# Performance work log

Measured on AMD Instinct MI355X. Metric: run time of the kernel, lower is better.

Reference implementation:

```python
import jax, jax.numpy as jnp
import numpy as np

B, L, D, H = 2, 2048, 1024, 16
DH = D // H
NEG = -10000.0

def setup_inputs() -> dict:
    key = jax.random.key(0)
    ks = jax.random.split(key, 6)
    scale = 1.0 / np.sqrt(D)
    inp = {
        "x": jax.random.normal(ks[0], (B, L, D), dtype=jnp.float32),
        "m": jnp.ones((B, L), dtype=jnp.int32),  # 1 = valid token, 0 = padded
        "Wq": jax.random.normal(ks[1], (D, D), dtype=jnp.float32) * scale,
        "bq": jnp.zeros((D,), dtype=jnp.float32),
        "Wk": jax.random.normal(ks[2], (D, D), dtype=jnp.float32) * scale,
        "bk": jnp.zeros((D,), dtype=jnp.float32),
        "Wv": jax.random.normal(ks[3], (D, D), dtype=jnp.float32) * scale,
        "bv": jnp.zeros((D,), dtype=jnp.float32),
        "Wp": jax.random.normal(ks[4], (D, D), dtype=jnp.float32) * scale,
        "bp": jnp.zeros((D,), dtype=jnp.float32),
    }
    return inp

def reference(x, m, Wq, bq, Wk, bk, Wv, bv, Wp, bp):
    # torch Linear: x @ W.T + b
    def heads(t):  # (B,L,D) -> (B,H,L,DH)
        return t.reshape(B, L, H, DH).transpose(0, 2, 1, 3)
    q = heads(x @ Wq.T + bq)
    k = heads(x @ Wk.T + bk)
    v = heads(x @ Wv.T + bv)
    att = jnp.einsum("bhqd,bhkd->bhqk", q, k) * (1.0 / np.sqrt(DH))  # (B,H,L,L)
    causal = jnp.tril(jnp.ones((L, L), dtype=bool))[None, None]       # (1,1,L,L)
    att = jnp.where(causal, att, NEG)
    # additive key-padding mask: 0 for valid, -10000 for padded keys
    pad = (1.0 - m.astype(att.dtype))[:, None, None, :] * NEG         # (B,1,1,L)
    att = att + pad
    att = jax.nn.softmax(att, axis=-1)
    y = jnp.einsum("bhqk,bhkd->bhqd", att, v)                          # (B,H,L,DH)
    y = y.transpose(0, 2, 1, 3).reshape(B, L, D)
    return y @ Wp.T + bp
```

## Files before the change

### kernel.cpp

```cpp
#include <hip/hip_runtime.h>
#include <hip/hip_bf16.h>

#define NB 2
#define NL 2048
#define ND 1024
#define NH 16
#define NDH 64
#define NM (NB*NL)

typedef unsigned short u16;
typedef __attribute__((ext_vector_type(8))) short short8;
typedef __attribute__((ext_vector_type(4))) float floatx4;

#define QSCALE 0.180336880f

__device__ __forceinline__ u16 f2bf(float f) {
  union { float f; unsigned int u; } v; v.f = f;
  unsigned int r = v.u + 0x7FFF + ((v.u >> 16) & 1);
  return (u16)(r >> 16);
}

__device__ __forceinline__ void async_cp16(const u16* lds, const u16* g) {
  __builtin_amdgcn_global_load_lds(
      (const __attribute__((address_space(1))) void*)g,
      (__attribute__((address_space(3))) void*)lds, 16, 0, 0);
}

__device__ __forceinline__ float dpp_xor1_f(float v) {
  return __int_as_float(__builtin_amdgcn_mov_dpp(__float_as_int(v), 0xB1, 0xF, 0xF, true));
}

__device__ __forceinline__ unsigned pk_bf16(float lo, float hi) {
  __hip_bfloat162 h2 = __float22bfloat162_rn(make_float2(lo, hi));
  return *(unsigned*)&h2;
}

__global__ __launch_bounds__(256)
void cvt_all(const float* __restrict__ wq, const float* __restrict__ wk,
             const float* __restrict__ wv, const float* __restrict__ wp,
             const float* __restrict__ x,
             u16* __restrict__ ow, u16* __restrict__ ox)
{
  const int per4 = ND * ND / 4;
  const int tot  = 4 * per4 + NM * ND / 4;
  for (int t = blockIdx.x * 256 + threadIdx.x; t < tot; t += gridDim.x * 256) {
    const float* src; uint2* dst; int off;
    if (t < 4 * per4) {
      int w = t >> 18; off = t & (per4 - 1);
      src = (w == 0) ? wq : (w == 1) ? wk : (w == 2) ? wv : wp;
      dst = (uint2*)(ow + (size_t)w * ND * ND);
    } else {
      off = t - 4 * per4; src = x; dst = (uint2*)ox;
    }
    float4 f = ((const float4*)src)[off];
    u16 h[4] = { f2bf(f.x), f2bf(f.y), f2bf(f.z), f2bf(f.w) };
    dst[off] = *(const uint2*)h;
  }
}

#define BM 128
#define BN 128
#define BK 32
#define LDT 32

__global__ __launch_bounds__(256)
void gemm_qkv(const u16* __restrict__ A, const u16* __restrict__ Wb,
              const float* __restrict__ bq, const float* __restrict__ bk,
              const float* __restrict__ bv,
              u16* __restrict__ Qb, u16* __restrict__ Kb, u16* __restrict__ Vb)
{
  const int n0g = blockIdx.x * BN;
  const int z   = n0g >> 10;
  const int n0  = n0g & 1023;
  const u16* W    = Wb + (size_t)z * ND * ND;
  const float* Bi = (z == 0) ? bq : (z == 1) ? bk : bv;
  u16* C          = (z == 0) ? Qb : (z == 1) ? Kb : Vb;
  const float sc  = (z == 0) ? QSCALE : 1.0f;

  const int m0 = blockIdx.y * BM;
  const int tid  = threadIdx.x;
  const int lane = tid & 63;
  const int wave = tid >> 6;
  const int wm = (wave >> 1) * 64;
  const int wn = (wave & 1) * 64;
  const int quad = lane >> 4;
  const int l16  = lane & 15;

  __shared__ u16 As[BM * LDT];
  __shared__ u16 Bs[BN * LDT];

  floatx4 acc[4][4];
#pragma unroll
  for (int i = 0; i < 4; ++i)
#pragma unroll
    for (int j = 0; j < 4; ++j)
      acc[i][j] = (floatx4){0.f, 0.f, 0.f, 0.f};

  for (int k0 = 0; k0 < ND; k0 += BK) {
#pragma unroll
    for (int it = 0; it < 2; ++it) {
      int idx = tid + it * 256;
      int rr  = idx >> 2;
      int c8  = (idx & 3) << 3;
      async_cp16(&Bs[idx * 8], &W[(size_t)(n0 + rr) * ND + k0 + c8]);
      async_cp16(&As[idx * 8], &A[(size_t)(m0 + rr) * ND + k0 + c8]);
    }
    __syncthreads();

    short8 af[4], bfr[4];
#pragma unroll
    for (int i = 0; i < 4; ++i)
      af[i] = *(const short8*)&As[(wm + i * 16 + l16) * LDT + quad * 8];
#pragma unroll
    for (int j = 0; j < 4; ++j)
      bfr[j] = *(const short8*)&Bs[(wn + j * 16 + l16) * LDT + quad * 8];

#pragma unroll
    for (int i = 0; i < 4; ++i)
#pragma unroll
      for (int j = 0; j < 4; ++j)
        acc[i][j] = __builtin_amdgcn_mfma_f32_16x16x32_bf16(af[i], bfr[j], acc[i][j], 0, 0, 0);
    __syncthreads();
  }

#pragma unroll
  for (int j = 0; j < 4; ++j) {
    const int ncol = n0 + wn + j * 16 + l16;
    const float bv2 = Bi[ncol];
#pragma unroll
    for (int i = 0; i < 4; ++i) {
      const int mbase = m0 + wm + i * 16 + quad * 4;
#pragma unroll
      for (int r2 = 0; r2 < 4; ++r2) {
        float v = (acc[i][j][r2] + bv2) * sc;
        C[(size_t)(mbase + r2) * ND + ncol] = f2bf(v);
      }
    }
  }
}

#define BN2 64

__global__ __launch_bounds__(256)
void gemm_proj(const u16* __restrict__ A, const u16* __restrict__ W,
               const float* __restrict__ Bi, float* __restrict__ C)
{
  const int n0 = blockIdx.x * BN2;
  const int m0 = blockIdx.y * BM;
  const int tid  = threadIdx.x;
  const int lane = tid & 63;
  const int wave = tid >> 6;
  const int wm = (wave >> 1) * 64;
  const int wn = (wave & 1) * 32;
  const int quad = lane >> 4;
  const int l16  = lane & 15;

  __shared__ u16 As[BM * LDT];
  __shared__ u16 Bs[BN2 * LDT];

  floatx4 acc[4][2];
#pragma unroll
  for (int i = 0; i < 4; ++i)
#pragma unroll
    for (int j = 0; j < 2; ++j)
      acc[i][j] = (floatx4){0.f, 0.f, 0.f, 0.f};

  for (int k0 = 0; k0 < ND; k0 += BK) {
#pragma unroll
    for (int it = 0; it < 2; ++it) {
      int idx = tid + it * 256;
      int rr  = idx >> 2;
      int c8  = (idx & 3) << 3;
      async_cp16(&As[idx * 8], &A[(size_t)(m0 + rr) * ND + k0 + c8]);
    }
    {
      int rr = tid >> 2, c8 = (tid & 3) << 3;
      async_cp16(&Bs[tid * 8], &W[(size_t)(n0 + rr) * ND + k0 + c8]);
    }
    __syncthreads();

    short8 af[4], bfr[2];
#pragma unroll
    for (int i = 0; i < 4; ++i)
      af[i] = *(const short8*)&As[(wm + i * 16 + l16) * LDT + quad * 8];
#pragma unroll
    for (int j = 0; j < 2; ++j)
      bfr[j] = *(const short8*)&Bs[(wn + j * 16 + l16) * LDT + quad * 8];

#pragma unroll
    for (int i = 0; i < 4; ++i)
#pragma unroll
      for (int j = 0; j < 2; ++j)
        acc[i][j] = __builtin_amdgcn_mfma_f32_16x16x32_bf16(af[i], bfr[j], acc[i][j], 0, 0, 0);
    __syncthreads();
  }

#pragma unroll
  for (int j = 0; j < 2; ++j) {
    const int ncol = n0 + wn + j * 16 + l16;
    const float bv2 = Bi[ncol];
#pragma unroll
    for (int i = 0; i < 4; ++i) {
      const int mbase = m0 + wm + i * 16 + quad * 4;
#pragma unroll
      for (int r2 = 0; r2 < 4; ++r2)
        C[(size_t)(mbase + r2) * ND + ncol] = acc[i][j][r2] + bv2;
    }
  }
}

#define TSTR 66
__global__ __launch_bounds__(256)
void vtrans(const u16* __restrict__ V, u16* __restrict__ VT)
{
  const int lt = blockIdx.x;
  const int bh = blockIdx.y;
  const int b = bh >> 4, h = bh & 15;
  const int l0 = lt * 64;
  const int tid = threadIdx.x;
  __shared__ u16 Ls[64][TSTR];
#pragma unroll
  for (int p = 0; p < 2; ++p) {
    int idx = tid + p * 256;
    int r = idx >> 3, c = (idx & 7) << 3;
    *(uint4*)&Ls[r][c] = *(const uint4*)&V[(size_t)(b * NL + l0 + r) * ND + h * NDH + c];
  }
  __syncthreads();
#pragma unroll
  for (int p = 0; p < 2; ++p) {
    int idx = tid + p * 256;
    int lg = idx & 7, d = idx >> 3;
    u16 tb[8];
#pragma unroll
    for (int e = 0; e < 8; ++e) tb[e] = Ls[lg * 8 + e][d];
    *(uint4*)&VT[((size_t)(b * NH + h) * NDH + d) * NL + l0 + lg * 8] = *(const uint4*)tb;
  }
}

#define KC 64
#define PSTR 72

__global__ __launch_bounds__(256)
void attn_mfma(const u16* __restrict__ Q, const u16* __restrict__ K,
               const u16* __restrict__ VT, const int* __restrict__ msk,
               u16* __restrict__ Y)
{
  const int t = blockIdx.x;
  const int r = t >> 8;
  const int xcd = t & 7;
  const int v = (t >> 3) & 31;
  const int bh = xcd * 4 + r;
  const int qt = (r == 0) ? v
               : (r == 1) ? 31 - v
               : (r == 2) ? ((v + 16) & 31)
                          : ((15 - v) & 31);
  const int b = bh >> 4;
  const int h = bh & 15;
  const int q0 = qt * 64;
  const int tid  = threadIdx.x;
  const int lane = tid & 63;
  const int wave = tid >> 6;
  const int wq   = wave * 16;
  const int quad = lane >> 4;
  const int l16  = lane & 15;

  __shared__ u16 Ks[KC * 64];
  __shared__ u16 Vt[NDH * 64];
  __shared__ u16 Ps[64][PSTR];
  __shared__ u16 Ms[NL];

  const int nchunks = qt + 1;

  for (int j = tid; j < nchunks * KC; j += 256) Ms[j] = (u16)(msk[b * NL + j] ? 1 : 0);

  const u16* Kbase  = K  + (size_t)b * NL * ND + h * NDH;
  const u16* VTbase = VT + (size_t)(b * NH + h) * NDH * NL;

  short8 qf[2];
#pragma unroll
  for (int kk = 0; kk < 2; ++kk)
    qf[kk] = *(const short8*)&Q[(size_t)(b * NL + q0 + wq + l16) * ND
                                + h * NDH + kk * 32 + quad * 8];

  short8 onesf;
  {
    const short ov = (l16 == 0) ? (short)0x3F80 : (short)0;
#pragma unroll
    for (int e = 0; e < 8; ++e) onesf[e] = ov;
  }

  floatx4 o[4];
#pragma unroll
  for (int ot = 0; ot < 4; ++ot) o[ot] = (floatx4){0.f, 0.f, 0.f, 0.f};
  floatx4 lacc = (floatx4){0.f, 0.f, 0.f, 0.f};

  const int odd = l16 & 1;
  const int sw  = l16 & 7;

  for (int kc = 0; kc < nchunks; ++kc) {
    const int k0 = kc * KC;

#pragma unroll
    for (int p = 0; p < 2; ++p) {
      int sl = tid + p * 256;
      int rr = sl >> 3;
      int ch = (sl & 7) ^ (rr & 7);
      async_cp16(&Ks[sl * 8], Kbase + (size_t)(k0 + rr) * ND + ch * 8);
      async_cp16(&Vt[sl * 8], VTbase + (size_t)rr * NL + k0 + ch * 8);
    }
    __syncthreads();

    floatx4 sc[4];
#pragma unroll
    for (int ct = 0; ct < 4; ++ct) {
      const u16* krow = &Ks[(ct * 16 + l16) * 64];
      short8 kf0 = *(const short8*)(krow + ((quad ^ sw) << 3));
      short8 kf1 = *(const short8*)(krow + (((4 | quad) ^ sw) << 3));
      floatx4 a = (floatx4){0.f, 0.f, 0.f, 0.f};
      a = __builtin_amdgcn_mfma_f32_16x16x32_bf16(qf[0], kf0, a, 0, 0, 0);
      a = __builtin_amdgcn_mfma_f32_16x16x32_bf16(qf[1], kf1, a, 0, 0, 0);
      sc[ct] = a;
    }

    const bool diag = (kc == qt);
    const int rowb = q0 + wq + quad * 4;
#pragma unroll
    for (int ct = 0; ct < 4; ++ct) {
      const int col = k0 + ct * 16 + l16;
      const float pmul = (float)Ms[col];
      float pv[4];
#pragma unroll
      for (int r2 = 0; r2 < 4; ++r2) {
        float p = pmul * __builtin_amdgcn_exp2f(sc[ct][r2]);
        if (diag) p = (col > rowb + r2) ? 0.f : p;
        pv[r2] = p;
      }
      float nb0 = dpp_xor1_f(pv[0]), nb1 = dpp_xor1_f(pv[1]);
      float nb2 = dpp_xor1_f(pv[2]), nb3 = dpp_xor1_f(pv[3]);
      const int colb  = ct * 16 + (l16 & ~1);
      const int row01 = wq + quad * 4 + odd;
      unsigned d01 = odd ? pk_bf16(nb1, pv[1]) : pk_bf16(pv[0], nb0);
      unsigned d23 = odd ? pk_bf16(nb3, pv[3]) : pk_bf16(pv[2], nb2);
      *(unsigned*)&Ps[row01][colb]     = d01;
      *(unsigned*)&Ps[row01 + 2][colb] = d23;
    }

#pragma unroll
    for (int kk = 0; kk < 2; ++kk) {
      short8 pf = *(const short8*)&Ps[wq + l16][kk * 32 + quad * 8];
#pragma unroll
      for (int ot = 0; ot < 4; ++ot) {
        const u16* vrow = &Vt[(ot * 16 + l16) * 64];
        short8 vf = *(const short8*)(vrow + ((((kk << 2) | quad) ^ sw) << 3));
        o[ot] = __builtin_amdgcn_mfma_f32_16x16x32_bf16(pf, vf, o[ot], 0, 0, 0);
      }
      lacc = __builtin_amdgcn_mfma_f32_16x16x32_bf16(pf, onesf, lacc, 0, 0, 0);
    }
    __syncthreads();
  }

  float inv[4];
#pragma unroll
  for (int r2 = 0; r2 < 4; ++r2) {
    const float l = __shfl(lacc[r2], quad << 4);
    inv[r2] = 1.0f / l;
  }
#pragma unroll
  for (int ot = 0; ot < 4; ++ot)
#pragma unroll
    for (int r2 = 0; r2 < 4; ++r2) {
      const int row = q0 + wq + quad * 4 + r2;
      Y[(size_t)(b * NL + row) * ND + h * NDH + ot * 16 + l16] = f2bf(o[ot][r2] * inv[r2]);
    }
}

extern "C" void kernel_launch(void* const* d_in, const int* in_sizes, int n_in,
                              void* d_out, int out_size, void* d_ws, size_t ws_size,
                              hipStream_t stream) {
  const float* x  = (const float*)d_in[0];
  const int*   m  = (const int*)d_in[1];
  const float* Wq = (const float*)d_in[2];
  const float* bq = (const float*)d_in[3];
  const float* Wk = (const float*)d_in[4];
  const float* bk = (const float*)d_in[5];
  const float* Wv = (const float*)d_in[6];
  const float* bv = (const float*)d_in[7];
  const float* Wp = (const float*)d_in[8];
  const float* bp = (const float*)d_in[9];
  float* out = (float*)d_out;

  const size_t per = (size_t)NM * ND;
  u16* Qb = (u16*)d_ws;
  u16* Kb = Qb + per;
  u16* Vb = Kb + per;
  u16* Wb = Vb + per;
  u16* Yb = Qb;
  u16* xb = (u16*)d_out;
  u16* VTb = xb + per;

  cvt_all<<<2048, 256, 0, stream>>>(Wq, Wk, Wv, Wp, x, Wb, xb);

  gemm_qkv<<<dim3(3 * ND / BN, NM / BM), 256, 0, stream>>>(
      xb, Wb, bq, bk, bv, Qb, Kb, Vb);

  vtrans<<<dim3(NL / 64, NB * NH), 256, 0, stream>>>(Vb, VTb);

  attn_mfma<<<1024, 256, 0, stream>>>(Qb, Kb, VTb, m, Yb);

  const u16* Wpb = Wb + 3 * (size_t)ND * ND;
  gemm_proj<<<dim3(ND / BN2, NM / BM), 256, 0, stream>>>(Yb, Wpb, bp, out);
}
```

Measured before the change: 195.5 us.

## Fuse V transpose into QKV GEMM epilogue, deepen proj K tile, stream mask

The QKV GEMM epilogue now writes the V projection directly in transposed head-major layout with packed 4-element stores, which removes the separate vtrans kernel and its extra read and write of V. The output projection GEMM doubles its K tile to 64, halving barrier count per K loop. The attention kernel drops the LDS mask staging, reads the mask from global per chunk, and splits the diagonal chunk out of the loop so the causal compare is specialised away. The transposed V writes are strided 8-byte stores, which may be less coalesced than the old transpose kernel's writes.

```diff
diff --git a/kernel.cpp b/kernel.cpp
--- a/kernel.cpp
+++ b/kernel.cpp
@@ -67,14 +67,13 @@
 void gemm_qkv(const u16* __restrict__ A, const u16* __restrict__ Wb,
               const float* __restrict__ bq, const float* __restrict__ bk,
               const float* __restrict__ bv,
-              u16* __restrict__ Qb, u16* __restrict__ Kb, u16* __restrict__ Vb)
+              u16* __restrict__ Qb, u16* __restrict__ Kb, u16* __restrict__ VTb)
 {
   const int n0g = blockIdx.x * BN;
   const int z   = n0g >> 10;
   const int n0  = n0g & 1023;
   const u16* W    = Wb + (size_t)z * ND * ND;
   const float* Bi = (z == 0) ? bq : (z == 1) ? bk : bv;
-  u16* C          = (z == 0) ? Qb : (z == 1) ? Kb : Vb;
   const float sc  = (z == 0) ? QSCALE : 1.0f;
 
   const int m0 = blockIdx.y * BM;
@@ -123,23 +122,43 @@
     __syncthreads();
   }
 
-#pragma unroll
-  for (int j = 0; j < 4; ++j) {
-    const int ncol = n0 + wn + j * 16 + l16;
-    const float bv2 = Bi[ncol];
-#pragma unroll
-    for (int i = 0; i < 4; ++i) {
-      const int mbase = m0 + wm + i * 16 + quad * 4;
-#pragma unroll
-      for (int r2 = 0; r2 < 4; ++r2) {
-        float v = (acc[i][j][r2] + bv2) * sc;
-        C[(size_t)(mbase + r2) * ND + ncol] = f2bf(v);
+  if (z == 2) {
+#pragma unroll
+    for (int j = 0; j < 4; ++j) {
+      const int ncol = n0 + wn + j * 16 + l16;
+      const int h2 = ncol >> 6, d = ncol & 63;
+      const float bv2 = Bi[ncol];
+#pragma unroll
+      for (int i = 0; i < 4; ++i) {
+        const int mbase = m0 + wm + i * 16 + quad * 4;
+        const int b2 = mbase >> 11, l = mbase & (NL - 1);
+        uint2 val;
+        val.x = pk_bf16(acc[i][j][0] + bv2, acc[i][j][1] + bv2);
+        val.y = pk_bf16(acc[i][j][2] + bv2, acc[i][j][3] + bv2);
+        *(uint2*)&VTb[((size_t)(b2 * NH + h2) * NDH + d) * NL + l] = val;
       }
     }
+  } else {
+    u16* C = (z == 0) ? Qb : Kb;
+#pragma unroll
+    for (int j = 0; j < 4; ++j) {
+      const int ncol = n0 + wn + j * 16 + l16;
+      const float bv2 = Bi[ncol];
+#pragma unroll
+      for (int i = 0; i < 4; ++i) {
+        const int mbase = m0 + wm + i * 16 + quad * 4;
+#pragma unroll
+        for (int r2 = 0; r2 < 4; ++r2) {
+          float v = (acc[i][j][r2] + bv2) * sc;
+          C[(size_t)(mbase + r2) * ND + ncol] = f2bf(v);
+        }
+      }
+    }
   }
 }
 
 #define BN2 64
+#define BK2 64
 
 __global__ __launch_bounds__(256)
 void gemm_proj(const u16* __restrict__ A, const u16* __restrict__ W,
@@ -155,8 +174,8 @@
   const int quad = lane >> 4;
   const int l16  = lane & 15;
 
-  __shared__ u16 As[BM * LDT];
-  __shared__ u16 Bs[BN2 * LDT];
+  __shared__ u16 As[BM * BK2];
+  __shared__ u16 Bs[BN2 * BK2];
 
   floatx4 acc[4][2];
 #pragma unroll
@@ -165,33 +184,38 @@
     for (int j = 0; j < 2; ++j)
       acc[i][j] = (floatx4){0.f, 0.f, 0.f, 0.f};
 
-  for (int k0 = 0; k0 < ND; k0 += BK) {
+  for (int k0 = 0; k0 < ND; k0 += BK2) {
+#pragma unroll
+    for (int it = 0; it < 4; ++it) {
+      int idx = tid + it * 256;
+      int rr  = idx >> 3;
+      int c8  = (idx & 7) << 3;
+      async_cp16(&As[idx * 8], &A[(size_t)(m0 + rr) * ND + k0 + c8]);
+    }
 #pragma unroll
     for (int it = 0; it < 2; ++it) {
       int idx = tid + it * 256;
-      int rr  = idx >> 2;
-      int c8  = (idx & 3) << 3;
-      async_cp16(&As[idx * 8], &A[(size_t)(m0 + rr) * ND + k0 + c8]);
-    }
-    {
-      int rr = tid >> 2, c8 = (tid & 3) << 3;
-      async_cp16(&Bs[tid * 8], &W[(size_t)(n0 + rr) * ND + k0 + c8]);
-    }
-    __syncthreads();
-
-    short8 af[4], bfr[2];
-#pragma unroll
-    for (int i = 0; i < 4; ++i)
-      af[i] = *(const short8*)&As[(wm + i * 16 + l16) * LDT + quad * 8];
-#pragma unroll
-    for (int j = 0; j < 2; ++j)
-      bfr[j] = *(const short8*)&Bs[(wn + j * 16 + l16) * LDT + quad * 8];
-
-#pragma unroll
-    for (int i = 0; i < 4; ++i)
+      int rr  = idx >> 3;
+      int c8  = (idx & 7) << 3;
+      async_cp16(&Bs[idx * 8], &W[(size_t)(n0 + rr) * ND + k0 + c8]);
+    }
+    __syncthreads();
+
+#pragma unroll
+    for (int kk = 0; kk < 2; ++kk) {
+      short8 af[4], bfr[2];
+#pragma unroll
+      for (int i = 0; i < 4; ++i)
+        af[i] = *(const short8*)&As[(wm + i * 16 + l16) * BK2 + kk * 32 + quad * 8];
 #pragma unroll
       for (int j = 0; j < 2; ++j)
-        acc[i][j] = __builtin_amdgcn_mfma_f32_16x16x32_bf16(af[i], bfr[j], acc[i][j], 0, 0, 0);
+        bfr[j] = *(const short8*)&Bs[(wn + j * 16 + l16) * BK2 + kk * 32 + quad * 8];
+#pragma unroll
+      for (int i = 0; i < 4; ++i)
+#pragma unroll
+        for (int j = 0; j < 2; ++j)
+          acc[i][j] = __builtin_amdgcn_mfma_f32_16x16x32_bf16(af[i], bfr[j], acc[i][j], 0, 0, 0);
+    }
     __syncthreads();
   }
 
@@ -206,34 +230,6 @@
       for (int r2 = 0; r2 < 4; ++r2)
         C[(size_t)(mbase + r2) * ND + ncol] = acc[i][j][r2] + bv2;
     }
-  }
-}
-
-#define TSTR 66
-__global__ __launch_bounds__(256)
-void vtrans(const u16* __restrict__ V, u16* __restrict__ VT)
-{
-  const int lt = blockIdx.x;
-  const int bh = blockIdx.y;
-  const int b = bh >> 4, h = bh & 15;
-  const int l0 = lt * 64;
-  const int tid = threadIdx.x;
-  __shared__ u16 Ls[64][TSTR];
-#pragma unroll
-  for (int p = 0; p < 2; ++p) {
-    int idx = tid + p * 256;
-    int r = idx >> 3, c = (idx & 7) << 3;
-    *(uint4*)&Ls[r][c] = *(const uint4*)&V[(size_t)(b * NL + l0 + r) * ND + h * NDH + c];
-  }
-  __syncthreads();
-#pragma unroll
-  for (int p = 0; p < 2; ++p) {
-    int idx = tid + p * 256;
-    int lg = idx & 7, d = idx >> 3;
-    u16 tb[8];
-#pragma unroll
-    for (int e = 0; e < 8; ++e) tb[e] = Ls[lg * 8 + e][d];
-    *(uint4*)&VT[((size_t)(b * NH + h) * NDH + d) * NL + l0 + lg * 8] = *(const uint4*)tb;
   }
 }
 
@@ -267,14 +263,10 @@
   __shared__ u16 Ks[KC * 64];
   __shared__ u16 Vt[NDH * 64];
   __shared__ u16 Ps[64][PSTR];
-  __shared__ u16 Ms[NL];
-
-  const int nchunks = qt + 1;
-
-  for (int j = tid; j < nchunks * KC; j += 256) Ms[j] = (u16)(msk[b * NL + j] ? 1 : 0);
 
   const u16* Kbase  = K  + (size_t)b * NL * ND + h * NDH;
   const u16* VTbase = VT + (size_t)(b * NH + h) * NDH * NL;
+  const int* mbase  = msk + b * NL;
 
   short8 qf[2];
 #pragma unroll
@@ -296,10 +288,9 @@
 
   const int odd = l16 & 1;
   const int sw  = l16 & 7;
-
-  for (int kc = 0; kc < nchunks; ++kc) {
-    const int k0 = kc * KC;
-
+  const int rowb = q0 + wq + quad * 4;
+
+  auto chunk_body = [&](int k0, bool diag) {
 #pragma unroll
     for (int p = 0; p < 2; ++p) {
       int sl = tid + p * 256;
@@ -309,6 +300,10 @@
       async_cp16(&Vt[sl * 8], VTbase + (size_t)rr * NL + k0 + ch * 8);
     }
     __syncthreads();
+
+    int mm[4];
+#pragma unroll
+    for (int ct = 0; ct < 4; ++ct) mm[ct] = mbase[k0 + ct * 16 + l16];
 
     floatx4 sc[4];
 #pragma unroll
@@ -322,17 +317,17 @@
       sc[ct] = a;
     }
 
-    const bool diag = (kc == qt);
-    const int rowb = q0 + wq + quad * 4;
 #pragma unroll
     for (int ct = 0; ct < 4; ++ct) {
-      const int col = k0 + ct * 16 + l16;
-      const float pmul = (float)Ms[col];
+      const float pmul = (float)mm[ct];
       float pv[4];
 #pragma unroll
       for (int r2 = 0; r2 < 4; ++r2) {
         float p = pmul * __builtin_amdgcn_exp2f(sc[ct][r2]);
-        if (diag) p = (col > rowb + r2) ? 0.f : p;
+        if (diag) {
+          const int col = k0 + ct * 16 + l16;
+          p = (col > rowb + r2) ? 0.f : p;
+        }
         pv[r2] = p;
       }
       float nb0 = dpp_xor1_f(pv[0]), nb1 = dpp_xor1_f(pv[1]);
@@ -357,7 +352,10 @@
       lacc = __builtin_amdgcn_mfma_f32_16x16x32_bf16(pf, onesf, lacc, 0, 0, 0);
     }
     __syncthreads();
-  }
+  };
+
+  for (int kc = 0; kc < qt; ++kc) chunk_body(kc * KC, false);
+  chunk_body(qt * KC, true);
 
   float inv[4];
 #pragma unroll
@@ -392,8 +390,7 @@
   const size_t per = (size_t)NM * ND;
   u16* Qb = (u16*)d_ws;
   u16* Kb = Qb + per;
-  u16* Vb = Kb + per;
-  u16* Wb = Vb + per;
+  u16* Wb = Kb + 2 * per;
   u16* Yb = Qb;
   u16* xb = (u16*)d_out;
   u16* VTb = xb + per;
@@ -401,9 +398,7 @@
   cvt_all<<<2048, 256, 0, stream>>>(Wq, Wk, Wv, Wp, x, Wb, xb);
 
   gemm_qkv<<<dim3(3 * ND / BN, NM / BM), 256, 0, stream>>>(
-      xb, Wb, bq, bk, bv, Qb, Kb, Vb);
-
-  vtrans<<<dim3(NL / 64, NB * NH), 256, 0, stream>>>(Vb, VTb);
+      xb, Wb, bq, bk, bv, Qb, Kb, VTb);
 
   attn_mfma<<<1024, 256, 0, stream>>>(Qb, Kb, VTb, m, Yb);
 
```

After: 207.1 us. 6.0% more time.

## Double GEMM K-tile to 64 with XOR-swizzled LDS and peel attention diagonal chunk

Applied to the files above, without the earlier changes.

Both the QKV and projection GEMMs now stage 64-wide K slices with an XOR-swizzled LDS layout. This halves the number of load/barrier iterations and is meant to avoid LDS bank conflicts on the fragment reads. In attention, the per-block mask staging into LDS is removed in favour of direct global loads of mask values per chunk. The diagonal chunk is peeled out of the loop so non-diagonal chunks skip the causal compare. LDS usage per GEMM block doubles, which may lower occupancy.

```diff
diff --git a/kernel.cpp b/kernel.cpp
--- a/kernel.cpp
+++ b/kernel.cpp
@@ -60,8 +60,7 @@
 
 #define BM 128
 #define BN 128
-#define BK 32
-#define LDT 32
+#define BKQ 64
 
 __global__ __launch_bounds__(256)
 void gemm_qkv(const u16* __restrict__ A, const u16* __restrict__ Wb,
@@ -85,9 +84,10 @@
   const int wn = (wave & 1) * 64;
   const int quad = lane >> 4;
   const int l16  = lane & 15;
-
-  __shared__ u16 As[BM * LDT];
-  __shared__ u16 Bs[BN * LDT];
+  const int sw   = l16 & 7;
+
+  __shared__ u16 As[BM * BKQ];
+  __shared__ u16 Bs[BN * BKQ];
 
   floatx4 acc[4][4];
 #pragma unroll
@@ -96,30 +96,33 @@
     for (int j = 0; j < 4; ++j)
       acc[i][j] = (floatx4){0.f, 0.f, 0.f, 0.f};
 
-  for (int k0 = 0; k0 < ND; k0 += BK) {
-#pragma unroll
-    for (int it = 0; it < 2; ++it) {
+  for (int k0 = 0; k0 < ND; k0 += BKQ) {
+#pragma unroll
+    for (int it = 0; it < 4; ++it) {
       int idx = tid + it * 256;
-      int rr  = idx >> 2;
-      int c8  = (idx & 3) << 3;
-      async_cp16(&Bs[idx * 8], &W[(size_t)(n0 + rr) * ND + k0 + c8]);
-      async_cp16(&As[idx * 8], &A[(size_t)(m0 + rr) * ND + k0 + c8]);
-    }
-    __syncthreads();
-
-    short8 af[4], bfr[4];
-#pragma unroll
-    for (int i = 0; i < 4; ++i)
-      af[i] = *(const short8*)&As[(wm + i * 16 + l16) * LDT + quad * 8];
-#pragma unroll
-    for (int j = 0; j < 4; ++j)
-      bfr[j] = *(const short8*)&Bs[(wn + j * 16 + l16) * LDT + quad * 8];
-
-#pragma unroll
-    for (int i = 0; i < 4; ++i)
+      int rr  = idx >> 3;
+      int ch  = (idx & 7) ^ (rr & 7);
+      async_cp16(&As[idx * 8], &A[(size_t)(m0 + rr) * ND + k0 + ch * 8]);
+      async_cp16(&Bs[idx * 8], &W[(size_t)(n0 + rr) * ND + k0 + ch * 8]);
+    }
+    __syncthreads();
+
+#pragma unroll
+    for (int kk = 0; kk < 2; ++kk) {
+      const int cq = ((kk << 2) | quad) ^ sw;
+      short8 af[4], bfr[4];
+#pragma unroll
+      for (int i = 0; i < 4; ++i)
+        af[i] = *(const short8*)&As[((wm + i * 16 + l16) * 8 + cq) * 8];
 #pragma unroll
       for (int j = 0; j < 4; ++j)
-        acc[i][j] = __builtin_amdgcn_mfma_f32_16x16x32_bf16(af[i], bfr[j], acc[i][j], 0, 0, 0);
+        bfr[j] = *(const short8*)&Bs[((wn + j * 16 + l16) * 8 + cq) * 8];
+#pragma unroll
+      for (int i = 0; i < 4; ++i)
+#pragma unroll
+        for (int j = 0; j < 4; ++j)
+          acc[i][j] = __builtin_amdgcn_mfma_f32_16x16x32_bf16(af[i], bfr[j], acc[i][j], 0, 0, 0);
+    }
     __syncthreads();
   }
 
@@ -140,6 +143,7 @@
 }
 
 #define BN2 64
+#define BK2 64
 
 __global__ __launch_bounds__(256)
 void gemm_proj(const u16* __restrict__ A, const u16* __restrict__ W,
@@ -154,9 +158,10 @@
   const int wn = (wave & 1) * 32;
   const int quad = lane >> 4;
   const int l16  = lane & 15;
-
-  __shared__ u16 As[BM * LDT];
-  __shared__ u16 Bs[BN2 * LDT];
+  const int sw   = l16 & 7;
+
+  __shared__ u16 As[BM * BK2];
+  __shared__ u16 Bs[BN2 * BK2];
 
   floatx4 acc[4][2];
 #pragma unroll
@@ -165,33 +170,39 @@
     for (int j = 0; j < 2; ++j)
       acc[i][j] = (floatx4){0.f, 0.f, 0.f, 0.f};
 
-  for (int k0 = 0; k0 < ND; k0 += BK) {
+  for (int k0 = 0; k0 < ND; k0 += BK2) {
+#pragma unroll
+    for (int it = 0; it < 4; ++it) {
+      int idx = tid + it * 256;
+      int rr  = idx >> 3;
+      int ch  = (idx & 7) ^ (rr & 7);
+      async_cp16(&As[idx * 8], &A[(size_t)(m0 + rr) * ND + k0 + ch * 8]);
+    }
 #pragma unroll
     for (int it = 0; it < 2; ++it) {
       int idx = tid + it * 256;
-      int rr  = idx >> 2;
-      int c8  = (idx & 3) << 3;
-      async_cp16(&As[idx * 8], &A[(size_t)(m0 + rr) * ND + k0 + c8]);
-    }
-    {
-      int rr = tid >> 2, c8 = (tid & 3) << 3;
-      async_cp16(&Bs[tid * 8], &W[(size_t)(n0 + rr) * ND + k0 + c8]);
-    }
-    __syncthreads();
-
-    short8 af[4], bfr[2];
-#pragma unroll
-    for (int i = 0; i < 4; ++i)
-      af[i] = *(const short8*)&As[(wm + i * 16 + l16) * LDT + quad * 8];
-#pragma unroll
-    for (int j = 0; j < 2; ++j)
-      bfr[j] = *(const short8*)&Bs[(wn + j * 16 + l16) * LDT + quad * 8];
-
-#pragma unroll
-    for (int i = 0; i < 4; ++i)
+      int rr  = idx >> 3;
+      int ch  = (idx & 7) ^ (rr & 7);
+      async_cp16(&Bs[idx * 8], &W[(size_t)(n0 + rr) * ND + k0 + ch * 8]);
+    }
+    __syncthreads();
+
+#pragma unroll
+    for (int kk = 0; kk < 2; ++kk) {
+      const int cq = ((kk << 2) | quad) ^ sw;
+      short8 af[4], bfr[2];
+#pragma unroll
+      for (int i = 0; i < 4; ++i)
+        af[i] = *(const short8*)&As[((wm + i * 16 + l16) * 8 + cq) * 8];
 #pragma unroll
       for (int j = 0; j < 2; ++j)
-        acc[i][j] = __builtin_amdgcn_mfma_f32_16x16x32_bf16(af[i], bfr[j], acc[i][j], 0, 0, 0);
+        bfr[j] = *(const short8*)&Bs[((wn + j * 16 + l16) * 8 + cq) * 8];
+#pragma unroll
+      for (int i = 0; i < 4; ++i)
+#pragma unroll
+        for (int j = 0; j < 2; ++j)
+          acc[i][j] = __builtin_amdgcn_mfma_f32_16x16x32_bf16(af[i], bfr[j], acc[i][j], 0, 0, 0);
+    }
     __syncthreads();
   }
 
@@ -267,14 +278,10 @@
   __shared__ u16 Ks[KC * 64];
   __shared__ u16 Vt[NDH * 64];
   __shared__ u16 Ps[64][PSTR];
-  __shared__ u16 Ms[NL];
-
-  const int nchunks = qt + 1;
-
-  for (int j = tid; j < nchunks * KC; j += 256) Ms[j] = (u16)(msk[b * NL + j] ? 1 : 0);
 
   const u16* Kbase  = K  + (size_t)b * NL * ND + h * NDH;
   const u16* VTbase = VT + (size_t)(b * NH + h) * NDH * NL;
+  const int* mbase  = msk + b * NL;
 
   short8 qf[2];
 #pragma unroll
@@ -296,10 +303,9 @@
 
   const int odd = l16 & 1;
   const int sw  = l16 & 7;
-
-  for (int kc = 0; kc < nchunks; ++kc) {
-    const int k0 = kc * KC;
-
+  const int rowb = q0 + wq + quad * 4;
+
+  auto chunk_body = [&](int k0, bool diag) {
 #pragma unroll
     for (int p = 0; p < 2; ++p) {
       int sl = tid + p * 256;
@@ -309,6 +315,10 @@
       async_cp16(&Vt[sl * 8], VTbase + (size_t)rr * NL + k0 + ch * 8);
     }
     __syncthreads();
+
+    int mm[4];
+#pragma unroll
+    for (int ct = 0; ct < 4; ++ct) mm[ct] = mbase[k0 + ct * 16 + l16];
 
     floatx4 sc[4];
 #pragma unroll
@@ -322,17 +332,17 @@
       sc[ct] = a;
     }
 
-    const bool diag = (kc == qt);
-    const int rowb = q0 + wq + quad * 4;
 #pragma unroll
     for (int ct = 0; ct < 4; ++ct) {
-      const int col = k0 + ct * 16 + l16;
-      const float pmul = (float)Ms[col];
+      const float pmul = (float)mm[ct];
       float pv[4];
 #pragma unroll
       for (int r2 = 0; r2 < 4; ++r2) {
         float p = pmul * __builtin_amdgcn_exp2f(sc[ct][r2]);
-        if (diag) p = (col > rowb + r2) ? 0.f : p;
+        if (diag) {
+          const int col = k0 + ct * 16 + l16;
+          p = (col > rowb + r2) ? 0.f : p;
+        }
         pv[r2] = p;
       }
       float nb0 = dpp_xor1_f(pv[0]), nb1 = dpp_xor1_f(pv[1]);
@@ -357,7 +367,10 @@
       lacc = __builtin_amdgcn_mfma_f32_16x16x32_bf16(pf, onesf, lacc, 0, 0, 0);
     }
     __syncthreads();
-  }
+  };
+
+  for (int kc = 0; kc < qt; ++kc) chunk_body(kc * KC, false);
+  chunk_body(qt * KC, true);
 
   float inv[4];
 #pragma unroll
```

Result: slower. 201.8 us (+3.2%).

## Split long causal query tiles across two blocks with a combine kernel

Applied to the files above, without the earlier changes.

Query tiles 16-31 of the causal attention are split into two key-range halves processed by separate blocks. Each half writes unnormalized bf16 partial outputs and row sums to scratch, and a new combine kernel adds them and normalizes. This balances work across 1536 blocks instead of 1024 uneven ones, reducing tail imbalance. The mask is now read straight from global memory per chunk instead of being staged in LDS. The cost is an extra launch, extra scratch traffic, and bf16 rounding of the partial sums.

```diff
diff --git a/kernel.cpp b/kernel.cpp
--- a/kernel.cpp
+++ b/kernel.cpp
@@ -13,6 +13,12 @@
 typedef __attribute__((ext_vector_type(4))) float floatx4;
 
 #define QSCALE 0.180336880f
+
+__device__ __forceinline__ float bf2f(u16 u) {
+  union { unsigned int ui; float f; } w;
+  w.ui = ((unsigned int)u) << 16;
+  return w.f;
+}
 
 __device__ __forceinline__ u16 f2bf(float f) {
   union { float f; unsigned int u; } v; v.f = f;
@@ -243,17 +249,26 @@
 __global__ __launch_bounds__(256)
 void attn_mfma(const u16* __restrict__ Q, const u16* __restrict__ K,
                const u16* __restrict__ VT, const int* __restrict__ msk,
-               u16* __restrict__ Y)
+               u16* __restrict__ Y, u16* __restrict__ PO, float* __restrict__ PL)
 {
   const int t = blockIdx.x;
   const int r = t >> 8;
-  const int xcd = t & 7;
-  const int v = (t >> 3) & 31;
-  const int bh = xcd * 4 + r;
-  const int qt = (r == 0) ? v
-               : (r == 1) ? 31 - v
-               : (r == 2) ? ((v + 16) & 31)
-                          : ((15 - v) & 31);
+  const int s = t & 255;
+  const int xcd = s & 7;
+  const int v = s >> 3;
+  const int bh = xcd * 4 + (v & 3);
+  const int p = v >> 2;
+
+  int qt, kc_lo, half = 0;
+  bool partial;
+  if (r == 0)      { qt = p;      kc_lo = 0;           partial = false; }
+  else if (r == 1) { qt = 15 - p; kc_lo = 0;           partial = false; }
+  else if (r == 2) { qt = 16 + p; kc_lo = 0;           partial = true; half = 0; }
+  else if (r == 3) { qt = 31 - p; kc_lo = (qt + 2) >> 1; partial = true; half = 1; }
+  else if (r == 4) { qt = 31 - p; kc_lo = 0;           partial = true; half = 0; }
+  else             { qt = 16 + p; kc_lo = (qt + 2) >> 1; partial = true; half = 1; }
+  const int kc_hi = (partial && half == 0) ? ((qt + 2) >> 1) - 1 : qt;
+
   const int b = bh >> 4;
   const int h = bh & 15;
   const int q0 = qt * 64;
@@ -267,14 +282,10 @@
   __shared__ u16 Ks[KC * 64];
   __shared__ u16 Vt[NDH * 64];
   __shared__ u16 Ps[64][PSTR];
-  __shared__ u16 Ms[NL];
-
-  const int nchunks = qt + 1;
-
-  for (int j = tid; j < nchunks * KC; j += 256) Ms[j] = (u16)(msk[b * NL + j] ? 1 : 0);
 
   const u16* Kbase  = K  + (size_t)b * NL * ND + h * NDH;
   const u16* VTbase = VT + (size_t)(b * NH + h) * NDH * NL;
+  const int* mbase  = msk + b * NL;
 
   short8 qf[2];
 #pragma unroll
@@ -296,13 +307,12 @@
 
   const int odd = l16 & 1;
   const int sw  = l16 & 7;
-
-  for (int kc = 0; kc < nchunks; ++kc) {
-    const int k0 = kc * KC;
-
-#pragma unroll
-    for (int p = 0; p < 2; ++p) {
-      int sl = tid + p * 256;
+  const int rowb = q0 + wq + quad * 4;
+
+  auto chunk_body = [&](int k0, bool diag) {
+#pragma unroll
+    for (int pp = 0; pp < 2; ++pp) {
+      int sl = tid + pp * 256;
       int rr = sl >> 3;
       int ch = (sl & 7) ^ (rr & 7);
       async_cp16(&Ks[sl * 8], Kbase + (size_t)(k0 + rr) * ND + ch * 8);
@@ -310,7 +320,11 @@
     }
     __syncthreads();
 
-    floatx4 sc[4];
+    int mm[4];
+#pragma unroll
+    for (int ct = 0; ct < 4; ++ct) mm[ct] = mbase[k0 + ct * 16 + l16];
+
+    floatx4 sc4[4];
 #pragma unroll
     for (int ct = 0; ct < 4; ++ct) {
       const u16* krow = &Ks[(ct * 16 + l16) * 64];
@@ -319,21 +333,21 @@
       floatx4 a = (floatx4){0.f, 0.f, 0.f, 0.f};
       a = __builtin_amdgcn_mfma_f32_16x16x32_bf16(qf[0], kf0, a, 0, 0, 0);
       a = __builtin_amdgcn_mfma_f32_16x16x32_bf16(qf[1], kf1, a, 0, 0, 0);
-      sc[ct] = a;
-    }
-
-    const bool diag = (kc == qt);
-    const int rowb = q0 + wq + quad * 4;
+      sc4[ct] = a;
+    }
+
 #pragma unroll
     for (int ct = 0; ct < 4; ++ct) {
-      const int col = k0 + ct * 16 + l16;
-      const float pmul = (float)Ms[col];
+      const float pmul = (float)mm[ct];
       float pv[4];
 #pragma unroll
       for (int r2 = 0; r2 < 4; ++r2) {
-        float p = pmul * __builtin_amdgcn_exp2f(sc[ct][r2]);
-        if (diag) p = (col > rowb + r2) ? 0.f : p;
-        pv[r2] = p;
+        float pr = pmul * __builtin_amdgcn_exp2f(sc4[ct][r2]);
+        if (diag) {
+          const int col = k0 + ct * 16 + l16;
+          pr = (col > rowb + r2) ? 0.f : pr;
+        }
+        pv[r2] = pr;
       }
       float nb0 = dpp_xor1_f(pv[0]), nb1 = dpp_xor1_f(pv[1]);
       float nb2 = dpp_xor1_f(pv[2]), nb3 = dpp_xor1_f(pv[3]);
@@ -357,21 +371,67 @@
       lacc = __builtin_amdgcn_mfma_f32_16x16x32_bf16(pf, onesf, lacc, 0, 0, 0);
     }
     __syncthreads();
-  }
-
-  float inv[4];
-#pragma unroll
-  for (int r2 = 0; r2 < 4; ++r2) {
-    const float l = __shfl(lacc[r2], quad << 4);
-    inv[r2] = 1.0f / l;
-  }
-#pragma unroll
-  for (int ot = 0; ot < 4; ++ot)
+  };
+
+  for (int kc = kc_lo; kc < kc_hi; ++kc) chunk_body(kc * KC, false);
+  chunk_body(kc_hi * KC, kc_hi == qt);
+
+  if (!partial) {
+    float inv[4];
 #pragma unroll
     for (int r2 = 0; r2 < 4; ++r2) {
-      const int row = q0 + wq + quad * 4 + r2;
-      Y[(size_t)(b * NL + row) * ND + h * NDH + ot * 16 + l16] = f2bf(o[ot][r2] * inv[r2]);
-    }
+      const float l = __shfl(lacc[r2], quad << 4);
+      inv[r2] = 1.0f / l;
+    }
+#pragma unroll
+    for (int ot = 0; ot < 4; ++ot)
+#pragma unroll
+      for (int r2 = 0; r2 < 4; ++r2) {
+        const int row = q0 + wq + quad * 4 + r2;
+        Y[(size_t)(b * NL + row) * ND + h * NDH + ot * 16 + l16] = f2bf(o[ot][r2] * inv[r2]);
+      }
+  } else {
+    const int slot = (bh * 16 + (qt - 16)) * 2 + half;
+    u16* po = PO + (size_t)slot * 4096;
+#pragma unroll
+    for (int ot = 0; ot < 4; ++ot)
+#pragma unroll
+      for (int r2 = 0; r2 < 4; ++r2)
+        po[(wq + quad * 4 + r2) * 64 + ot * 16 + l16] = f2bf(o[ot][r2]);
+    if (l16 == 0) {
+#pragma unroll
+      for (int r2 = 0; r2 < 4; ++r2)
+        PL[slot * 64 + wq + quad * 4 + r2] = lacc[r2];
+    }
+  }
+}
+
+__global__ __launch_bounds__(256)
+void attn_combine(const u16* __restrict__ PO, const float* __restrict__ PL,
+                  u16* __restrict__ Y)
+{
+  const int tt = blockIdx.x;
+  const int bh = tt >> 4, qx = tt & 15, qt = 16 + qx;
+  const int b = bh >> 4, h = bh & 15;
+  const int tid = threadIdx.x;
+  const int row = tid >> 2, cg = (tid & 3) << 4;
+  const int sl0 = (bh * 16 + qx) * 2;
+  const float l = PL[sl0 * 64 + row] + PL[(sl0 + 1) * 64 + row];
+  const float inv = 1.0f / l;
+  const u16* p0 = PO + (size_t)sl0 * 4096 + row * 64 + cg;
+  const u16* p1 = p0 + 4096;
+  u16* y = Y + (size_t)(b * NL + qt * 64 + row) * ND + h * NDH + cg;
+  uint4 a0 = *(const uint4*)p0, a1 = *(const uint4*)(p0 + 8);
+  uint4 b0 = *(const uint4*)p1, b1 = *(const uint4*)(p1 + 8);
+  const u16* ap = (const u16*)&a0; const u16* bp = (const u16*)&b0;
+  u16 outv[16];
+#pragma unroll
+  for (int e = 0; e < 8; ++e) outv[e] = f2bf((bf2f(ap[e]) + bf2f(bp[e])) * inv);
+  ap = (const u16*)&a1; bp = (const u16*)&b1;
+#pragma unroll
+  for (int e = 0; e < 8; ++e) outv[8 + e] = f2bf((bf2f(ap[e]) + bf2f(bp[e])) * inv);
+  *(uint4*)y = *(const uint4*)outv;
+  *(uint4*)(y + 8) = *(const uint4*)(outv + 8);
 }
 
 extern "C" void kernel_launch(void* const* d_in, const int* in_sizes, int n_in,
@@ -397,6 +457,8 @@
   u16* Yb = Qb;
   u16* xb = (u16*)d_out;
   u16* VTb = xb + per;
+  u16* PO = xb;
+  float* PL = (float*)Vb;
 
   cvt_all<<<2048, 256, 0, stream>>>(Wq, Wk, Wv, Wp, x, Wb, xb);
 
@@ -405,7 +467,9 @@
 
   vtrans<<<dim3(NL / 64, NB * NH), 256, 0, stream>>>(Vb, VTb);
 
-  attn_mfma<<<1024, 256, 0, stream>>>(Qb, Kb, VTb, m, Yb);
+  attn_mfma<<<1536, 256, 0, stream>>>(Qb, Kb, VTb, m, Yb, PO, PL);
+
+  attn_combine<<<512, 256, 0, stream>>>(PO, PL, Yb);
 
   const u16* Wpb = Wb + 3 * (size_t)ND * ND;
   gemm_proj<<<dim3(ND / BN2, NM / BM), 256, 0, stream>>>(Yb, Wpb, bp, out);
```

After: 192.5 us. No clear change (-1.5%).
